# Kernel optimization log

Measured on AMD Instinct MI355X. Metric: run time of the kernel, lower is better.

The kernel has to match this reference:

```python
import jax, jax.numpy as jnp
import numpy as np

B, N, F_IN, H = 32, 1024, 64, 24


def setup_inputs() -> dict:
    key = jax.random.key(0)
    k1, k2 = jax.random.split(key)
    xt = jax.random.normal(k1, (B, N, F_IN), dtype=jnp.float32)
    # nn.Linear init scale ~ 1/sqrt(in_feats)
    W = jax.random.normal(k2, (F_IN, H), dtype=jnp.float32) / jnp.sqrt(jnp.float32(F_IN))
    b = jnp.zeros((H,), dtype=jnp.float32)
    return {"xt": xt, "W": W, "b": b}


def reference(xt, W, b):
    # Z = relu(Linear(xt)) : (B, N, H)
    Z = jax.nn.relu(jnp.einsum("bnf,fh->bnh", xt, W) + b)
    # raw similarity adjacency (B, N, N)
    A = jnp.einsum("bnh,bmh->bnm", Z, Z)
    # symmetric softmax
    A = 0.5 * (jax.nn.softmax(A, axis=-1) + jax.nn.softmax(A, axis=-2))
    # self loops
    A = A + jnp.eye(N, dtype=A.dtype)[None, :, :]
    # Kipf normalization D^-1/2 A D^-1/2 (diag bmm == row/col broadcast scale)
    degree = jnp.clip(jnp.sum(A, axis=-1), 1e-6, None)  # (B, N)
    d_inv_sqrt = degree ** -0.5
    A_normalized = A * d_inv_sqrt[:, :, None] * d_inv_sqrt[:, None, :]
    return A_normalized
```

## Files before the change

### kernel.cpp

```cpp
#include <hip/hip_runtime.h>

#define BB 32
#define NN 1024
#define FIN 64
#define HH 24
#define SQRT_LOG2E 1.2011224087864498f

typedef __attribute__((ext_vector_type(8))) short short8;
typedef __attribute__((ext_vector_type(4))) float floatx4;

static __device__ inline unsigned short bf16_rtne(float f) {
    unsigned u = __float_as_uint(f);
    unsigned r = u + 0x7FFFu + ((u >> 16) & 1u);
    return (unsigned short)(r >> 16);
}

__global__ void k_z(const float* __restrict__ xt, const float* __restrict__ W,
                    const float* __restrict__ bias, unsigned short* __restrict__ Zhl) {
    __shared__ float Wl[FIN * HH];
    int t = threadIdx.x;
    for (int i = t; i < FIN * HH; i += 256) Wl[i] = W[i];
    __syncthreads();

    int row = blockIdx.x * 256 + t;

    const float* xr = xt + (size_t)row * FIN;
    float x[FIN];
    #pragma unroll
    for (int k4 = 0; k4 < FIN / 4; ++k4) {
        float4 v = reinterpret_cast<const float4*>(xr)[k4];
        x[4 * k4 + 0] = v.x; x[4 * k4 + 1] = v.y;
        x[4 * k4 + 2] = v.z; x[4 * k4 + 3] = v.w;
    }

    unsigned short u[64];
    #pragma unroll
    for (int i = 0; i < 64; ++i) u[i] = 0;

    #pragma unroll
    for (int hg = 0; hg < HH / 4; ++hg) {
        float4 acc = reinterpret_cast<const float4*>(bias)[hg];
        #pragma unroll
        for (int k = 0; k < FIN; ++k) {
            float4 w = *reinterpret_cast<const float4*>(&Wl[k * HH + hg * 4]);
            acc.x += x[k] * w.x; acc.y += x[k] * w.y;
            acc.z += x[k] * w.z; acc.w += x[k] * w.w;
        }
        float zs[4] = { fmaxf(acc.x, 0.f) * SQRT_LOG2E, fmaxf(acc.y, 0.f) * SQRT_LOG2E,
                        fmaxf(acc.z, 0.f) * SQRT_LOG2E, fmaxf(acc.w, 0.f) * SQRT_LOG2E };
        #pragma unroll
        for (int j = 0; j < 4; ++j) {
            int h = hg * 4 + j;
            unsigned short hb = bf16_rtne(zs[j]);
            float hf = __uint_as_float((unsigned)hb << 16);
            u[h] = hb;
            u[32 + h] = bf16_rtne(zs[j] - hf);
        }
    }

    unsigned short* dst = Zhl + ((size_t)row << 6);
    #pragma unroll
    for (int i = 0; i < 8; ++i)
        reinterpret_cast<uint4*>(dst)[i] = *reinterpret_cast<const uint4*>(&u[i * 8]);
}


#define STAGE_CHUNK(m0)                                                                  \
    for (int i = t; i < 1024; i += 256) {                                                \
        int row_ = i >> 3, c_ = i & 7;                                                   \
        uint4 v_ = *reinterpret_cast<const uint4*>(                                      \
            Zhl + (((size_t)b * NN + (m0) + row_) << 6) + (c_ << 3));                    \
        *reinterpret_cast<uint4*>(&Bs[(((c_ << 7) + (row_ ^ c_)) << 3)]) = v_;           \
    }

#define LOAD_A_FRAGS()                                                                   \
    const unsigned short* arow_ = Zhl + (((size_t)b * NN + n0w + r15) << 6) + (g << 3);  \
    short8 ah = *reinterpret_cast<const short8*>(arow_);                                 \
    short8 al = *reinterpret_cast<const short8*>(arow_ + 32);

#define B_FRAGS(mt)                                                                      \
    int roff = (mt) * 16 + r15;                                                          \
    short8 bh = *reinterpret_cast<const short8*>(&Bs[((g << 7) + (roff ^ g)) << 3]);     \
    short8 bl = *reinterpret_cast<const short8*>(                                        \
        &Bs[(((g + 4) << 7) + (roff ^ (g + 4))) << 3]);                                  \
    floatx4 acc = {0.f, 0.f, 0.f, 0.f};                                                  \
    acc = __builtin_amdgcn_mfma_f32_16x16x32_bf16(ah, bh, acc, 0, 0, 0);                 \
    acc = __builtin_amdgcn_mfma_f32_16x16x32_bf16(ah, bl, acc, 0, 0, 0);                 \
    acc = __builtin_amdgcn_mfma_f32_16x16x32_bf16(al, bh, acc, 0, 0, 0);

__global__ __launch_bounds__(256) void k_rowsum(
        const unsigned short* __restrict__ Zhl, float* __restrict__ ps) {
    __shared__ unsigned short Bs[128 * 64];
    int t = threadIdx.x, lane = t & 63, w = t >> 6;
    int r15 = lane & 15, g = lane >> 4;
    int b = blockIdx.z;
    int n0w = blockIdx.x * 64 + w * 16;
    int mbase = blockIdx.y * 256;

    LOAD_A_FRAGS();

    float s[4] = {0.f, 0.f, 0.f, 0.f};

    #pragma unroll
    for (int ch = 0; ch < 2; ++ch) {
        __syncthreads();
        STAGE_CHUNK(mbase + ch * 128);
        __syncthreads();
        #pragma unroll
        for (int mt = 0; mt < 8; ++mt) {
            B_FRAGS(mt);
            s[0] += __builtin_amdgcn_exp2f(acc[0]);
            s[1] += __builtin_amdgcn_exp2f(acc[1]);
            s[2] += __builtin_amdgcn_exp2f(acc[2]);
            s[3] += __builtin_amdgcn_exp2f(acc[3]);
        }
    }

    #pragma unroll
    for (int off = 1; off < 16; off <<= 1)
        #pragma unroll
        for (int k = 0; k < 4; ++k) s[k] += __shfl_xor(s[k], off, 64);

    if (r15 == 0) {
        size_t base = ((size_t)blockIdx.y * BB + b) * NN + n0w + g * 4;
        #pragma unroll
        for (int k = 0; k < 4; ++k) ps[base + k] = s[k];
    }
}

__global__ void k_rowfin(const float* __restrict__ ps, float* __restrict__ L) {
    int i = blockIdx.x * 256 + threadIdx.x;
    float s = ps[i] + ps[32768 + i] + ps[65536 + i] + ps[98304 + i];
    L[i] = __builtin_amdgcn_logf(s);
}

__global__ __launch_bounds__(256) void k_colsum(
        const unsigned short* __restrict__ Zhl, const float* __restrict__ L,
        float* __restrict__ pc) {
    __shared__ unsigned short Bs[128 * 64];
    __shared__ float Ls[128];
    int t = threadIdx.x, lane = t & 63, w = t >> 6;
    int r15 = lane & 15, g = lane >> 4;
    int b = blockIdx.z;
    int n0w = blockIdx.x * 64 + w * 16;
    int mbase = blockIdx.y * 256;

    LOAD_A_FRAGS();

    float s[4] = {0.f, 0.f, 0.f, 0.f};

    #pragma unroll
    for (int ch = 0; ch < 2; ++ch) {
        int m0 = mbase + ch * 128;
        __syncthreads();
        STAGE_CHUNK(m0);
        if (t < 128) Ls[t] = L[(size_t)b * NN + m0 + t];
        __syncthreads();
        #pragma unroll
        for (int mt = 0; mt < 8; ++mt) {
            B_FRAGS(mt);
            float lm = Ls[roff];
            s[0] += __builtin_amdgcn_exp2f(acc[0] - lm);
            s[1] += __builtin_amdgcn_exp2f(acc[1] - lm);
            s[2] += __builtin_amdgcn_exp2f(acc[2] - lm);
            s[3] += __builtin_amdgcn_exp2f(acc[3] - lm);
        }
    }

    #pragma unroll
    for (int off = 1; off < 16; off <<= 1)
        #pragma unroll
        for (int k = 0; k < 4; ++k) s[k] += __shfl_xor(s[k], off, 64);

    if (r15 == 0) {
        size_t base = ((size_t)blockIdx.y * BB + b) * NN + n0w + g * 4;
        #pragma unroll
        for (int k = 0; k < 4; ++k) pc[base + k] = s[k];
    }
}

__global__ void k_colfin(const float* __restrict__ pc, float* __restrict__ dinv) {
    int i = blockIdx.x * 256 + threadIdx.x;
    float s = pc[i] + pc[32768 + i] + pc[65536 + i] + pc[98304 + i];
    dinv[i] = rsqrtf(1.5f + 0.5f * s);
}

__global__ __launch_bounds__(256) void k_out(
        const unsigned short* __restrict__ Zhl, const float* __restrict__ L,
        const float* __restrict__ dinv, float* __restrict__ out) {
    __shared__ unsigned short Bs[128 * 64];
    __shared__ float Ls[128], dvS[128];
    int t = threadIdx.x, lane = t & 63, w = t >> 6;
    int r15 = lane & 15, g = lane >> 4;
    int b = blockIdx.z;
    int n0w = blockIdx.x * 64 + w * 16;
    int mbase = blockIdx.y * 256;

    LOAD_A_FRAGS();

    float en4[4], dvn4[4];
    #pragma unroll
    for (int k = 0; k < 4; ++k) {
        int n = n0w + g * 4 + k;
        en4[k]  = __builtin_amdgcn_exp2f(-1.0f - L[(size_t)b * NN + n]);
        dvn4[k] = dinv[(size_t)b * NN + n];
    }

    #pragma unroll
    for (int ch = 0; ch < 2; ++ch) {
        int m0 = mbase + ch * 128;
        __syncthreads();
        STAGE_CHUNK(m0);
        if (t < 128) {
            Ls[t]  = L[(size_t)b * NN + m0 + t];
            dvS[t] = dinv[(size_t)b * NN + m0 + t];
        }
        __syncthreads();
        #pragma unroll
        for (int mt = 0; mt < 8; ++mt) {
            B_FRAGS(mt);
            float em  = __builtin_amdgcn_exp2f(-1.0f - Ls[roff]);
            float dvm = dvS[roff];
            int mg = m0 + roff;
            #pragma unroll
            for (int k = 0; k < 4; ++k) {
                int ng = n0w + g * 4 + k;
                float v = __builtin_amdgcn_exp2f(acc[k]) * (en4[k] + em);
                if (ng == mg) v += 1.0f;
                out[((size_t)b * NN + ng) * NN + mg] = v * dvn4[k] * dvm;
            }
        }
    }
}

extern "C" void kernel_launch(void* const* d_in, const int* in_sizes, int n_in,
                              void* d_out, int out_size, void* d_ws, size_t ws_size,
                              hipStream_t stream) {
    const float* xt   = (const float*)d_in[0];
    const float* W    = (const float*)d_in[1];
    const float* bias = (const float*)d_in[2];
    float* out = (float*)d_out;
    float* ws  = (float*)d_ws;

    unsigned short* Zhl = (unsigned short*)ws;
    float* L    = ws + 1048576;
    float* dinv = ws + 1048576 + 32768;
    float* ps   = ws + 1048576 + 65536;
    float* pc   = ws + 1048576 + 65536 + 131072;

    k_z<<<dim3(BB * NN / 256), dim3(256), 0, stream>>>(xt, W, bias, Zhl);
    k_rowsum<<<dim3(16, 4, BB), dim3(256), 0, stream>>>(Zhl, ps);
    k_rowfin<<<dim3(128), dim3(256), 0, stream>>>(ps, L);
    k_colsum<<<dim3(16, 4, BB), dim3(256), 0, stream>>>(Zhl, L, pc);
    k_colfin<<<dim3(128), dim3(256), 0, stream>>>(pc, dinv);
    k_out<<<dim3(16, 4, BB), dim3(256), 0, stream>>>(Zhl, L, dinv, out);
}
```

Before: 87.50 us.

## Swap MFMA operands for row-contiguous float4 stores and fold finalize kernels

Swaps the MFMA operand order so each lane's four accumulator values land on four consecutive m columns of one output row. This lets k_out write float4 vectors instead of scattered scalar stores. The separate row/col finalize kernels are removed: partial sums are combined and inverted inside the consuming kernels, replacing log/exp with reciprocal multiplies, and the cross-lane reductions shrink to two shuffles. This trades two launches and scalar stores for redundant partial-sum reads in every block.

Result: faster. 83.10 us (-5.0%).

```diff
diff --git a/kernel.cpp b/kernel.cpp
--- a/kernel.cpp
+++ b/kernel.cpp
@@ -73,33 +73,33 @@
         *reinterpret_cast<uint4*>(&Bs[(((c_ << 7) + (row_ ^ c_)) << 3)]) = v_;           \
     }
 
-#define LOAD_A_FRAGS()                                                                   \
-    const unsigned short* arow_ = Zhl + (((size_t)b * NN + n0w + r15) << 6) + (g << 3);  \
-    short8 ah = *reinterpret_cast<const short8*>(arow_);                                 \
-    short8 al = *reinterpret_cast<const short8*>(arow_ + 32);
-
-#define B_FRAGS(mt)                                                                      \
+#define LOAD_N_FRAGS()                                                                   \
+    const unsigned short* nrow_ = Zhl + (((size_t)b * NN + n0w + r15) << 6) + (g << 3);  \
+    short8 nh = *reinterpret_cast<const short8*>(nrow_);                                 \
+    short8 nl = *reinterpret_cast<const short8*>(nrow_ + 32);
+
+#define MFMA_TILE(mt)                                                                    \
     int roff = (mt) * 16 + r15;                                                          \
-    short8 bh = *reinterpret_cast<const short8*>(&Bs[((g << 7) + (roff ^ g)) << 3]);     \
-    short8 bl = *reinterpret_cast<const short8*>(                                        \
+    short8 mh = *reinterpret_cast<const short8*>(&Bs[((g << 7) + (roff ^ g)) << 3]);     \
+    short8 ml = *reinterpret_cast<const short8*>(                                        \
         &Bs[(((g + 4) << 7) + (roff ^ (g + 4))) << 3]);                                  \
     floatx4 acc = {0.f, 0.f, 0.f, 0.f};                                                  \
-    acc = __builtin_amdgcn_mfma_f32_16x16x32_bf16(ah, bh, acc, 0, 0, 0);                 \
-    acc = __builtin_amdgcn_mfma_f32_16x16x32_bf16(ah, bl, acc, 0, 0, 0);                 \
-    acc = __builtin_amdgcn_mfma_f32_16x16x32_bf16(al, bh, acc, 0, 0, 0);
+    acc = __builtin_amdgcn_mfma_f32_16x16x32_bf16(mh, nh, acc, 0, 0, 0);                 \
+    acc = __builtin_amdgcn_mfma_f32_16x16x32_bf16(mh, nl, acc, 0, 0, 0);                 \
+    acc = __builtin_amdgcn_mfma_f32_16x16x32_bf16(ml, nh, acc, 0, 0, 0);
 
 __global__ __launch_bounds__(256) void k_rowsum(
         const unsigned short* __restrict__ Zhl, float* __restrict__ ps) {
     __shared__ unsigned short Bs[128 * 64];
-    int t = threadIdx.x, lane = t & 63, w = t >> 6;
+    int t = threadIdx.x, lane = t & 63;
     int r15 = lane & 15, g = lane >> 4;
     int b = blockIdx.z;
-    int n0w = blockIdx.x * 64 + w * 16;
+    int n0w = blockIdx.x * 64 + (t >> 6) * 16;
     int mbase = blockIdx.y * 256;
 
-    LOAD_A_FRAGS();
-
-    float s[4] = {0.f, 0.f, 0.f, 0.f};
+    LOAD_N_FRAGS();
+
+    float s = 0.f;
 
     #pragma unroll
     for (int ch = 0; ch < 2; ++ch) {
@@ -108,127 +108,116 @@
         __syncthreads();
         #pragma unroll
         for (int mt = 0; mt < 8; ++mt) {
-            B_FRAGS(mt);
-            s[0] += __builtin_amdgcn_exp2f(acc[0]);
-            s[1] += __builtin_amdgcn_exp2f(acc[1]);
-            s[2] += __builtin_amdgcn_exp2f(acc[2]);
-            s[3] += __builtin_amdgcn_exp2f(acc[3]);
-        }
-    }
-
-    #pragma unroll
-    for (int off = 1; off < 16; off <<= 1)
-        #pragma unroll
-        for (int k = 0; k < 4; ++k) s[k] += __shfl_xor(s[k], off, 64);
-
-    if (r15 == 0) {
-        size_t base = ((size_t)blockIdx.y * BB + b) * NN + n0w + g * 4;
-        #pragma unroll
-        for (int k = 0; k < 4; ++k) ps[base + k] = s[k];
-    }
-}
-
-__global__ void k_rowfin(const float* __restrict__ ps, float* __restrict__ L) {
-    int i = blockIdx.x * 256 + threadIdx.x;
-    float s = ps[i] + ps[32768 + i] + ps[65536 + i] + ps[98304 + i];
-    L[i] = __builtin_amdgcn_logf(s);
+            MFMA_TILE(mt);
+            s += __builtin_amdgcn_exp2f(acc[0]) + __builtin_amdgcn_exp2f(acc[1])
+               + __builtin_amdgcn_exp2f(acc[2]) + __builtin_amdgcn_exp2f(acc[3]);
+        }
+    }
+
+    s += __shfl_xor(s, 16, 64);
+    s += __shfl_xor(s, 32, 64);
+    if (g == 0)
+        ps[((size_t)blockIdx.y * BB + b) * NN + n0w + r15] = s;
 }
 
 __global__ __launch_bounds__(256) void k_colsum(
-        const unsigned short* __restrict__ Zhl, const float* __restrict__ L,
+        const unsigned short* __restrict__ Zhl, const float* __restrict__ ps,
         float* __restrict__ pc) {
     __shared__ unsigned short Bs[128 * 64];
-    __shared__ float Ls[128];
-    int t = threadIdx.x, lane = t & 63, w = t >> 6;
+    __shared__ float rmS[256];
+    int t = threadIdx.x, lane = t & 63;
     int r15 = lane & 15, g = lane >> 4;
     int b = blockIdx.z;
-    int n0w = blockIdx.x * 64 + w * 16;
+    int n0w = blockIdx.x * 64 + (t >> 6) * 16;
     int mbase = blockIdx.y * 256;
 
-    LOAD_A_FRAGS();
-
-    float s[4] = {0.f, 0.f, 0.f, 0.f};
+    {
+        size_t o = (size_t)b * NN + mbase + t;
+        float sm = ps[o] + ps[32768 + o] + ps[65536 + o] + ps[98304 + o];
+        rmS[t] = 1.0f / sm;
+    }
+
+    LOAD_N_FRAGS();
+
+    float c = 0.f;
+
+    #pragma unroll
+    for (int ch = 0; ch < 2; ++ch) {
+        __syncthreads();
+        STAGE_CHUNK(mbase + ch * 128);
+        __syncthreads();
+        #pragma unroll
+        for (int mt = 0; mt < 8; ++mt) {
+            MFMA_TILE(mt);
+            float4 rm4 = *reinterpret_cast<const float4*>(&rmS[ch * 128 + mt * 16 + g * 4]);
+            c += __builtin_amdgcn_exp2f(acc[0]) * rm4.x + __builtin_amdgcn_exp2f(acc[1]) * rm4.y
+               + __builtin_amdgcn_exp2f(acc[2]) * rm4.z + __builtin_amdgcn_exp2f(acc[3]) * rm4.w;
+        }
+    }
+
+    c += __shfl_xor(c, 16, 64);
+    c += __shfl_xor(c, 32, 64);
+    if (g == 0)
+        pc[((size_t)blockIdx.y * BB + b) * NN + n0w + r15] = c;
+}
+
+__global__ __launch_bounds__(256) void k_out(
+        const unsigned short* __restrict__ Zhl, const float* __restrict__ ps,
+        const float* __restrict__ pc, float* __restrict__ out) {
+    __shared__ unsigned short Bs[128 * 64];
+    __shared__ float emS[256], dvmS[256];
+    int t = threadIdx.x, lane = t & 63;
+    int r15 = lane & 15, g = lane >> 4;
+    int b = blockIdx.z;
+    int n0w = blockIdx.x * 64 + (t >> 6) * 16;
+    int mbase = blockIdx.y * 256;
+
+    {
+        size_t o = (size_t)b * NN + mbase + t;
+        float sm = ps[o] + ps[32768 + o] + ps[65536 + o] + ps[98304 + o];
+        float cm = pc[o] + pc[32768 + o] + pc[65536 + o] + pc[98304 + o];
+        emS[t]  = 0.5f / sm;
+        dvmS[t] = rsqrtf(1.5f + 0.5f * cm);
+    }
+
+    int n = n0w + r15;
+    float en, dvn;
+    {
+        size_t o = (size_t)b * NN + n;
+        float sn = ps[o] + ps[32768 + o] + ps[65536 + o] + ps[98304 + o];
+        float cn = pc[o] + pc[32768 + o] + pc[65536 + o] + pc[98304 + o];
+        en  = 0.5f / sn;
+        dvn = rsqrtf(1.5f + 0.5f * cn);
+    }
+
+    LOAD_N_FRAGS();
+
+    float* orow = out + ((size_t)b * NN + n) * NN;
 
     #pragma unroll
     for (int ch = 0; ch < 2; ++ch) {
         int m0 = mbase + ch * 128;
         __syncthreads();
         STAGE_CHUNK(m0);
-        if (t < 128) Ls[t] = L[(size_t)b * NN + m0 + t];
         __syncthreads();
         #pragma unroll
         for (int mt = 0; mt < 8; ++mt) {
-            B_FRAGS(mt);
-            float lm = Ls[roff];
-            s[0] += __builtin_amdgcn_exp2f(acc[0] - lm);
-            s[1] += __builtin_amdgcn_exp2f(acc[1] - lm);
-            s[2] += __builtin_amdgcn_exp2f(acc[2] - lm);
-            s[3] += __builtin_amdgcn_exp2f(acc[3] - lm);
-        }
-    }
-
-    #pragma unroll
-    for (int off = 1; off < 16; off <<= 1)
-        #pragma unroll
-        for (int k = 0; k < 4; ++k) s[k] += __shfl_xor(s[k], off, 64);
-
-    if (r15 == 0) {
-        size_t base = ((size_t)blockIdx.y * BB + b) * NN + n0w + g * 4;
-        #pragma unroll
-        for (int k = 0; k < 4; ++k) pc[base + k] = s[k];
-    }
-}
-
-__global__ void k_colfin(const float* __restrict__ pc, float* __restrict__ dinv) {
-    int i = blockIdx.x * 256 + threadIdx.x;
-    float s = pc[i] + pc[32768 + i] + pc[65536 + i] + pc[98304 + i];
-    dinv[i] = rsqrtf(1.5f + 0.5f * s);
-}
-
-__global__ __launch_bounds__(256) void k_out(
-        const unsigned short* __restrict__ Zhl, const float* __restrict__ L,
-        const float* __restrict__ dinv, float* __restrict__ out) {
-    __shared__ unsigned short Bs[128 * 64];
-    __shared__ float Ls[128], dvS[128];
-    int t = threadIdx.x, lane = t & 63, w = t >> 6;
-    int r15 = lane & 15, g = lane >> 4;
-    int b = blockIdx.z;
-    int n0w = blockIdx.x * 64 + w * 16;
-    int mbase = blockIdx.y * 256;
-
-    LOAD_A_FRAGS();
-
-    float en4[4], dvn4[4];
-    #pragma unroll
-    for (int k = 0; k < 4; ++k) {
-        int n = n0w + g * 4 + k;
-        en4[k]  = __builtin_amdgcn_exp2f(-1.0f - L[(size_t)b * NN + n]);
-        dvn4[k] = dinv[(size_t)b * NN + n];
-    }
-
-    #pragma unroll
-    for (int ch = 0; ch < 2; ++ch) {
-        int m0 = mbase + ch * 128;
-        __syncthreads();
-        STAGE_CHUNK(m0);
-        if (t < 128) {
-            Ls[t]  = L[(size_t)b * NN + m0 + t];
-            dvS[t] = dinv[(size_t)b * NN + m0 + t];
-        }
-        __syncthreads();
-        #pragma unroll
-        for (int mt = 0; mt < 8; ++mt) {
-            B_FRAGS(mt);
-            float em  = __builtin_amdgcn_exp2f(-1.0f - Ls[roff]);
-            float dvm = dvS[roff];
-            int mg = m0 + roff;
-            #pragma unroll
-            for (int k = 0; k < 4; ++k) {
-                int ng = n0w + g * 4 + k;
-                float v = __builtin_amdgcn_exp2f(acc[k]) * (en4[k] + em);
-                if (ng == mg) v += 1.0f;
-                out[((size_t)b * NN + ng) * NN + mg] = v * dvn4[k] * dvm;
-            }
+            MFMA_TILE(mt);
+            int mq = ch * 128 + mt * 16 + g * 4;
+            float4 em4 = *reinterpret_cast<const float4*>(&emS[mq]);
+            float4 dv4 = *reinterpret_cast<const float4*>(&dvmS[mq]);
+            int mg = mbase + mq;
+            float4 o;
+            float w0 = dvn * dv4.x, w1 = dvn * dv4.y, w2 = dvn * dv4.z, w3 = dvn * dv4.w;
+            o.x = __builtin_amdgcn_exp2f(acc[0]) * (en + em4.x) * w0;
+            o.y = __builtin_amdgcn_exp2f(acc[1]) * (en + em4.y) * w1;
+            o.z = __builtin_amdgcn_exp2f(acc[2]) * (en + em4.z) * w2;
+            o.w = __builtin_amdgcn_exp2f(acc[3]) * (en + em4.w) * w3;
+            if (n == mg + 0) o.x += w0;
+            if (n == mg + 1) o.y += w1;
+            if (n == mg + 2) o.z += w2;
+            if (n == mg + 3) o.w += w3;
+            *reinterpret_cast<float4*>(orow + mg) = o;
         }
     }
 }
@@ -243,15 +232,11 @@
     float* ws  = (float*)d_ws;
 
     unsigned short* Zhl = (unsigned short*)ws;
-    float* L    = ws + 1048576;
-    float* dinv = ws + 1048576 + 32768;
-    float* ps   = ws + 1048576 + 65536;
-    float* pc   = ws + 1048576 + 65536 + 131072;
+    float* ps = ws + 1048576;
+    float* pc = ws + 1048576 + 131072;
 
     k_z<<<dim3(BB * NN / 256), dim3(256), 0, stream>>>(xt, W, bias, Zhl);
     k_rowsum<<<dim3(16, 4, BB), dim3(256), 0, stream>>>(Zhl, ps);
-    k_rowfin<<<dim3(128), dim3(256), 0, stream>>>(ps, L);
-    k_colsum<<<dim3(16, 4, BB), dim3(256), 0, stream>>>(Zhl, L, pc);
-    k_colfin<<<dim3(128), dim3(256), 0, stream>>>(pc, dinv);
-    k_out<<<dim3(16, 4, BB), dim3(256), 0, stream>>>(Zhl, L, dinv, out);
-}
+    k_colsum<<<dim3(16, 4, BB), dim3(256), 0, stream>>>(Zhl, ps, pc);
+    k_out<<<dim3(16, 4, BB), dim3(256), 0, stream>>>(Zhl, ps, pc, out);
+}
```
